# Kernel tuning notes

Hardware: AMD Instinct MI355X
Metric: run time of the kernel (lower is better)

Reference implementation:

```python
import jax, jax.numpy as jnp
import numpy as np

N, D, H, C, ED, E = 50000, 128, 8, 16, 16, 800000  # nodes, model dim, heads, head dim, edge dim, edges

def _layer_norm(x, g, b, eps=1e-5):
    mu = x.mean(-1, keepdims=True)
    var = ((x - mu) ** 2).mean(-1, keepdims=True)
    return (x - mu) * jax.lax.rsqrt(var + eps) * g + b

def setup_inputs() -> dict:
    key = jax.random.key(0)
    ks = jax.random.split(key, 24)
    s = 0.05
    inp = {
        'x': jax.random.normal(ks[0], (N, D), jnp.float32),
        'edge_index': jax.random.randint(ks[1], (2, E), 0, N, jnp.int32),
        'edge_attr': jax.random.normal(ks[2], (E, ED), jnp.float32),
        # TransformerConv params (Linear convention: y = x @ W + b)
        'wq': s * jax.random.normal(ks[3], (D, H * C)), 'bq': s * jax.random.normal(ks[4], (H * C,)),
        'wk': s * jax.random.normal(ks[5], (D, H * C)), 'bk': s * jax.random.normal(ks[6], (H * C,)),
        'wv': s * jax.random.normal(ks[7], (D, H * C)), 'bv': s * jax.random.normal(ks[8], (H * C,)),
        'we': s * jax.random.normal(ks[9], (ED, H * C)),            # lin_edge, bias=False
        'wskip': s * jax.random.normal(ks[10], (D, H * C)), 'bskip': s * jax.random.normal(ks[11], (H * C,)),
        'wbeta': s * jax.random.normal(ks[12], (3 * H * C, 1)),     # lin_beta, bias=False
        # norms
        'ln1_g': 1.0 + s * jax.random.normal(ks[13], (D,)), 'ln1_b': s * jax.random.normal(ks[14], (D,)),
        'ln2_g': 1.0 + s * jax.random.normal(ks[15], (D,)), 'ln2_b': s * jax.random.normal(ks[16], (D,)),
        # FFN
        'w1': s * jax.random.normal(ks[17], (D, 2 * D)), 'b1': s * jax.random.normal(ks[18], (2 * D,)),
        'w2': s * jax.random.normal(ks[19], (2 * D, D)), 'b2': s * jax.random.normal(ks[20], (D,)),
    }
    return inp

def reference(x, edge_index, edge_attr, wq, bq, wk, bk, wv, bv, we, wskip, bskip, wbeta,
              ln1_g, ln1_b, ln2_g, ln2_b, w1, b1, w2, b2):
    src, dst = edge_index[0], edge_index[1]  # message flows src (j) -> dst (i)
    # --- pre-norm + TransformerConv (beta=True, concat=True, eval-mode dropout=identity) ---
    xn = _layer_norm(x, ln1_g, ln1_b)
    q = (xn @ wq + bq).reshape(N, H, C)
    k = (xn @ wk + bk).reshape(N, H, C)
    v = (xn @ wv + bv).reshape(N, H, C)
    e = (edge_attr @ we).reshape(E, H, C)
    kj = k[src] + e                                     # [E,H,C]
    alpha = (q[dst] * kj).sum(-1) / jnp.sqrt(jnp.float32(C))  # [E,H]
    # segment softmax over incoming edges per destination node
    m = jax.ops.segment_max(alpha, dst, num_segments=N)        # [N,H]
    ea = jnp.exp(alpha - m[dst])
    denom = jax.ops.segment_sum(ea, dst, num_segments=N)
    alpha = ea / (denom[dst] + 1e-16)
    msg = (v[src] + e) * alpha[..., None]               # [E,H,C]
    out = jax.ops.segment_sum(msg, dst, num_segments=N).reshape(N, H * C)
    # beta-gated skip
    x_r = xn @ wskip + bskip
    beta = jax.nn.sigmoid(jnp.concatenate([out, x_r, out - x_r], axis=-1) @ wbeta)  # [N,1]
    out = beta * x_r + (1.0 - beta) * out
    x = x + out
    # --- pre-norm FFN ---
    h = _layer_norm(x, ln2_g, ln2_b)
    h = jax.nn.gelu(h @ w1 + b1, approximate=False) @ w2 + b2
    return x + h
```

## Files before the change

kernel.cpp:

```cpp
#include <hip/hip_runtime.h>
#include <math.h>

#define N_NODES 50000
#define D_MODEL 128
#define N_HEADS 8
#define HEAD_C 16
#define E_DIM 16
#define N_EDGES 800000

typedef __attribute__((ext_vector_type(8))) short bf16x8;
typedef __attribute__((ext_vector_type(4))) float f32x4;

__device__ inline ushort f2bf(float f) {
    unsigned u = __float_as_uint(f);
    unsigned r = (u + 0x7fffu + ((u >> 16) & 1u)) >> 16;
    return (ushort)r;
}
__device__ inline float bf2f(ushort h) { return __uint_as_float(((unsigned)h) << 16); }
__device__ inline uint pack2(float a, float b) {
    return (uint)f2bf(a) | ((uint)f2bf(b) << 16);
}

__global__ void prep_weights(const float* __restrict__ wq, const float* __restrict__ wk,
                             const float* __restrict__ wv, const float* __restrict__ wsk,
                             const float* __restrict__ bq, const float* __restrict__ bk,
                             const float* __restrict__ bv, const float* __restrict__ bsk,
                             const float* __restrict__ w1, const float* __restrict__ w2,
                             ushort* __restrict__ wqkvsT, float* __restrict__ bqkvs,
                             ushort* __restrict__ w1T, ushort* __restrict__ w2T)
{
    int idx = blockIdx.x * 256 + threadIdx.x;
    {
        int m = idx >> 7, kk = idx & 127;
        int b = m >> 7, ch = m & 127;
        const float* src = (b == 0) ? wq : (b == 1) ? wk : (b == 2) ? wv : wsk;
        wqkvsT[idx] = f2bf(src[kk * 128 + ch]);
    }
    if (idx < 256 * 128) {
        int m = idx >> 7, k = idx & 127;
        w1T[idx] = f2bf(w1[k * 256 + m]);
    }
    if (idx < 128 * 256) {
        int m = idx >> 8, k = idx & 255;
        w2T[idx] = f2bf(w2[k * 128 + m]);
    }
    if (idx < 512) {
        int b = idx >> 7, ch = idx & 127;
        const float* bb = (b == 0) ? bq : (b == 1) ? bk : (b == 2) ? bv : bsk;
        bqkvs[idx] = bb[ch];
    }
}

__global__ void ln_kernel(const float* __restrict__ in, const float* __restrict__ g,
                          const float* __restrict__ b, ushort* __restrict__ out, int n)
{
    int node = blockIdx.x * 4 + (threadIdx.x >> 6);
    int lane = threadIdx.x & 63;
    if (node >= n) return;
    size_t base = (size_t)node * D_MODEL;
    float v0 = in[base + lane];
    float v1 = in[base + lane + 64];
    float s  = v0 + v1;
    float ss = v0 * v0 + v1 * v1;
    #pragma unroll
    for (int off = 32; off > 0; off >>= 1) {
        s  += __shfl_xor(s,  off, 64);
        ss += __shfl_xor(ss, off, 64);
    }
    float mu  = s * (1.0f / 128.0f);
    float var = ss * (1.0f / 128.0f) - mu * mu;
    float rs  = rsqrtf(var + 1e-5f);
    out[base + lane]      = f2bf((v0 - mu) * rs * g[lane]      + b[lane]);
    out[base + lane + 64] = f2bf((v1 - mu) * rs * g[lane + 64] + b[lane + 64]);
}

__global__ __launch_bounds__(256) void mfma_gemm(
    const ushort* __restrict__ A, const ushort* __restrict__ WT,
    const float* __restrict__ bias, const float* __restrict__ addsrc,
    void* __restrict__ Y, int nrows, int K, int M, int act, int outf32)
{
    __shared__ __align__(16) ushort Al[128 * 128];
    __shared__ __align__(16) ushort Wl[64 * 128];
    int tid = threadIdx.x;
    int wv = tid >> 6, lane = tid & 63;
    int row0 = blockIdx.x * 128;
    int col0 = blockIdx.y * 64;

    f32x4 acc[2][4];
    #pragma unroll
    for (int i = 0; i < 2; ++i)
        #pragma unroll
        for (int j = 0; j < 4; ++j) acc[i][j] = (f32x4){0.f, 0.f, 0.f, 0.f};

    for (int kc = 0; kc < K; kc += 128) {
        __syncthreads();
        #pragma unroll
        for (int i = 0; i < 8; ++i) {
            int c = tid + i * 256;
            int r = c >> 4, c16 = c & 15;
            int gr = row0 + r;
            ulonglong2 val = {0ull, 0ull};
            if (gr < nrows) val = *(const ulonglong2*)(A + (size_t)gr * K + kc + c16 * 8);
            int byte = r * 256 + ((c16 * 16) ^ ((r & 7) << 4));
            *(ulonglong2*)((char*)Al + byte) = val;
        }
        #pragma unroll
        for (int i = 0; i < 4; ++i) {
            int c = tid + i * 256;
            int r = c >> 4, c16 = c & 15;
            ulonglong2 val = *(const ulonglong2*)(WT + (size_t)(col0 + r) * K + kc + c16 * 8);
            int byte = r * 256 + ((c16 * 16) ^ ((r & 7) << 4));
            *(ulonglong2*)((char*)Wl + byte) = val;
        }
        __syncthreads();
        #pragma unroll
        for (int ks = 0; ks < 4; ++ks) {
            bf16x8 af[2], bfr[4];
            #pragma unroll
            for (int rt = 0; rt < 2; ++rt) {
                int r = wv * 32 + rt * 16 + (lane & 15);
                int byte = r * 256 + ((ks * 64 + (lane >> 4) * 16) ^ ((r & 7) << 4));
                af[rt] = *(const bf16x8*)((const char*)Al + byte);
            }
            #pragma unroll
            for (int ct = 0; ct < 4; ++ct) {
                int r = ct * 16 + (lane & 15);
                int byte = r * 256 + ((ks * 64 + (lane >> 4) * 16) ^ ((r & 7) << 4));
                bfr[ct] = *(const bf16x8*)((const char*)Wl + byte);
            }
            #pragma unroll
            for (int rt = 0; rt < 2; ++rt)
                #pragma unroll
                for (int ct = 0; ct < 4; ++ct)
                    acc[rt][ct] = __builtin_amdgcn_mfma_f32_16x16x32_bf16(
                        af[rt], bfr[ct], acc[rt][ct], 0, 0, 0);
        }
    }
    #pragma unroll
    for (int rt = 0; rt < 2; ++rt) {
        #pragma unroll
        for (int ct = 0; ct < 4; ++ct) {
            int gcol = col0 + ct * 16 + (lane & 15);
            float bv = bias[gcol];
            #pragma unroll
            for (int r = 0; r < 4; ++r) {
                int grow = row0 + wv * 32 + rt * 16 + (lane >> 4) * 4 + r;
                if (grow >= nrows) continue;
                float val = acc[rt][ct][r] + bv;
                if (act == 1)
                    val = 0.5f * val * (1.0f + erff(val * 0.70710678118654752f));
                size_t idx = (size_t)grow * M + gcol;
                if (outf32) {
                    float* Yf = (float*)Y;
                    if (addsrc) val += addsrc[idx];
                    Yf[idx] = val;
                } else {
                    ((ushort*)Y)[idx] = f2bf(val);
                }
            }
        }
    }
}

__global__ void hist_kernel(const int* __restrict__ dst, int* __restrict__ deg)
{
    int e = blockIdx.x * 256 + threadIdx.x;
    if (e < N_EDGES) atomicAdd(&deg[dst[e]], 1);
}

__global__ void scan1_kernel(const int* __restrict__ deg, int* __restrict__ off,
                             int* __restrict__ bsum)
{
    __shared__ int sm[256];
    int i = blockIdx.x * 256 + threadIdx.x;
    int v = (i < N_NODES) ? deg[i] : 0;
    sm[threadIdx.x] = v;
    __syncthreads();
    #pragma unroll
    for (int d = 1; d < 256; d <<= 1) {
        int t = (threadIdx.x >= d) ? sm[threadIdx.x - d] : 0;
        __syncthreads();
        sm[threadIdx.x] += t;
        __syncthreads();
    }
    if (i < N_NODES) off[i] = sm[threadIdx.x] - v;
    if (threadIdx.x == 255) bsum[blockIdx.x] = sm[255];
}

__global__ void scan2_kernel(int* __restrict__ bsum, int nb)
{
    __shared__ int sm[256];
    int v = (threadIdx.x < nb) ? bsum[threadIdx.x] : 0;
    sm[threadIdx.x] = v;
    __syncthreads();
    #pragma unroll
    for (int d = 1; d < 256; d <<= 1) {
        int t = (threadIdx.x >= d) ? sm[threadIdx.x - d] : 0;
        __syncthreads();
        sm[threadIdx.x] += t;
        __syncthreads();
    }
    if (threadIdx.x < nb) bsum[threadIdx.x] = sm[threadIdx.x] - v;
}

__global__ void scan3_kernel(int* __restrict__ off, const int* __restrict__ bsum,
                             int* __restrict__ cursor)
{
    int i = blockIdx.x * 256 + threadIdx.x;
    if (i < N_NODES) {
        int o = off[i] + bsum[blockIdx.x];
        off[i] = o;
        cursor[i] = o;
    }
}

__global__ void scatter_kernel(const int* __restrict__ dst, const int* __restrict__ src,
                               const float* __restrict__ eattr, int* __restrict__ cursor,
                               int* __restrict__ src_s, ushort* __restrict__ eattr_s)
{
    int e = blockIdx.x * 256 + threadIdx.x;
    if (e < N_EDGES) {
        int p = atomicAdd(&cursor[dst[e]], 1);
        src_s[p] = src[e];
        const float4* s4 = (const float4*)(eattr + (size_t)e * E_DIM);
        float4 f0 = s4[0], f1 = s4[1], f2 = s4[2], f3 = s4[3];
        uint4 u0, u1;
        u0.x = pack2(f0.x, f0.y); u0.y = pack2(f0.z, f0.w);
        u0.z = pack2(f1.x, f1.y); u0.w = pack2(f1.z, f1.w);
        u1.x = pack2(f2.x, f2.y); u1.y = pack2(f2.z, f2.w);
        u1.z = pack2(f3.x, f3.y); u1.w = pack2(f3.z, f3.w);
        uint4* d4 = (uint4*)(eattr_s + (size_t)p * E_DIM);
        d4[0] = u0; d4[1] = u1;
    }
}

#define ATTN_STEP(P, S, A0, A1, E0, E1) do {                                         \
    int sv_ = src_s[P];                                                              \
    uint eap_ = *(const uint*)(eattr_s + (size_t)(P) * E_DIM + j2);                  \
    float ea0_ = bf2f((ushort)eap_), ea1_ = bf2f((ushort)(eap_ >> 16));              \
    size_t sb_ = (size_t)sv_ * 512;                                                  \
    uint kp_ = *(const uint*)(qkvs + sb_ + 128 + 2 * lane);                          \
    uint vp_ = *(const uint*)(qkvs + sb_ + 256 + 2 * lane);                          \
    float p_ = q0 * bf2f((ushort)kp_) + q1 * bf2f((ushort)(kp_ >> 16))               \
             + ea0_ * qp0 + ea1_ * qp1;                                              \
    p_ += __shfl_xor(p_, 1, 64);                                                     \
    p_ += __shfl_xor(p_, 2, 64);                                                     \
    p_ += __shfl_xor(p_, 4, 64);                                                     \
    float w_ = __expf(fminf(p_ * 0.25f, 60.f));                                      \
    S  += w_;                                                                        \
    A0 += w_ * bf2f((ushort)vp_);                                                    \
    A1 += w_ * bf2f((ushort)(vp_ >> 16));                                            \
    E0 += w_ * ea0_;                                                                 \
    E1 += w_ * ea1_;                                                                 \
} while (0)

__global__ void node_attn(const ushort* __restrict__ qkvs, const float* __restrict__ x,
                          const float* __restrict__ we, const float* __restrict__ wbeta,
                          const int* __restrict__ off, const int* __restrict__ deg,
                          const int* __restrict__ src_s, const ushort* __restrict__ eattr_s,
                          float* __restrict__ xnew)
{
    __shared__ float wl[E_DIM * 128];
    __shared__ float weT[128 * 17];
    __shared__ float sc4[4][128];
    for (int t = threadIdx.x; t < E_DIM * 32; t += 256)
        *(float4*)&wl[t * 4] = *(const float4*)&we[t * 4];
    for (int t = threadIdx.x; t < E_DIM * 128; t += 256) {
        int j = t >> 7, ch = t & 127;
        weT[ch * 17 + j] = we[t];
    }
    __syncthreads();

    int nl   = threadIdx.x >> 6;
    int node = blockIdx.x * 4 + nl;
    int lane = threadIdx.x & 63;
    if (node >= N_NODES) return;

    int j2 = (lane & 7) * 2;
    int hb = (lane >> 3) * 16;

    size_t nb = (size_t)node * 512;
    uint qp = *(const uint*)(qkvs + nb + 2 * lane);
    float q0 = bf2f((ushort)qp), q1 = bf2f((ushort)(qp >> 16));

    sc4[nl][2 * lane]     = q0;
    sc4[nl][2 * lane + 1] = q1;
    float qp0 = 0.f, qp1 = 0.f;
    #pragma unroll
    for (int c = 0; c < 16; ++c) {
        float qc = sc4[nl][hb + c];
        qp0 += qc * weT[(hb + c) * 17 + j2];
        qp1 += qc * weT[(hb + c) * 17 + j2 + 1];
    }

    float SA = 0.f, A0a = 0.f, A1a = 0.f, E0a = 0.f, E1a = 0.f;
    float SB = 0.f, A0b = 0.f, A1b = 0.f, E0b = 0.f, E1b = 0.f;

    int o = off[node], dg = deg[node];
    int i = 0;
    for (; i + 2 <= dg; i += 2) {
        ATTN_STEP(o + i,     SA, A0a, A1a, E0a, E1a);
        ATTN_STEP(o + i + 1, SB, A0b, A1b, E0b, E1b);
    }
    if (i < dg)
        ATTN_STEP(o + i, SA, A0a, A1a, E0a, E1a);

    float S  = SA + SB;
    float A0 = A0a + A0b, A1 = A1a + A1b;
    float E0 = E0a + E0b, E1 = E1a + E1b;

    sc4[nl][2 * lane]     = E0;
    sc4[nl][2 * lane + 1] = E1;
    float ep0 = 0.f, ep1 = 0.f;
    #pragma unroll
    for (int j = 0; j < 16; ++j) {
        float es = sc4[nl][hb + j];
        ep0 += es * wl[j * 128 + 2 * lane];
        ep1 += es * wl[j * 128 + 2 * lane + 1];
    }

    float rinv = 1.f / (S + 1e-16f);
    float o0 = (A0 + ep0) * rinv;
    float o1 = (A1 + ep1) * rinv;

    uint xrp = *(const uint*)(qkvs + nb + 384 + 2 * lane);
    float xr0 = bf2f((ushort)xrp), xr1 = bf2f((ushort)(xrp >> 16));
    float2 wb0 = *(const float2*)&wbeta[2 * lane];
    float2 wb1 = *(const float2*)&wbeta[128 + 2 * lane];
    float2 wb2 = *(const float2*)&wbeta[256 + 2 * lane];
    float dot = o0 * wb0.x + o1 * wb0.y + xr0 * wb1.x + xr1 * wb1.y
              + (o0 - xr0) * wb2.x + (o1 - xr1) * wb2.y;
    #pragma unroll
    for (int w = 32; w > 0; w >>= 1) dot += __shfl_xor(dot, w, 64);
    float beta = 1.f / (1.f + __expf(-dot));

    size_t xb = (size_t)node * D_MODEL + 2 * lane;
    float2 xv = *(const float2*)&x[xb];
    float2 outv;
    outv.x = xv.x + beta * xr0 + (1.f - beta) * o0;
    outv.y = xv.y + beta * xr1 + (1.f - beta) * o1;
    *(float2*)&xnew[xb] = outv;
}

extern "C" void kernel_launch(void* const* d_in, const int* in_sizes, int n_in,
                              void* d_out, int out_size, void* d_ws, size_t ws_size,
                              hipStream_t stream)
{
    const float* x     = (const float*)d_in[0];
    const int*   eidx  = (const int*)  d_in[1];
    const float* eattr = (const float*)d_in[2];
    const float* wq  = (const float*)d_in[3];  const float* bq  = (const float*)d_in[4];
    const float* wk  = (const float*)d_in[5];  const float* bk  = (const float*)d_in[6];
    const float* wv  = (const float*)d_in[7];  const float* bv  = (const float*)d_in[8];
    const float* we  = (const float*)d_in[9];
    const float* wsk = (const float*)d_in[10]; const float* bsk = (const float*)d_in[11];
    const float* wbeta = (const float*)d_in[12];
    const float* ln1g = (const float*)d_in[13]; const float* ln1b = (const float*)d_in[14];
    const float* ln2g = (const float*)d_in[15]; const float* ln2b = (const float*)d_in[16];
    const float* w1 = (const float*)d_in[17]; const float* b1 = (const float*)d_in[18];
    const float* w2 = (const float*)d_in[19]; const float* b2 = (const float*)d_in[20];
    const int* srcp = eidx;
    const int* dstp = eidx + N_EDGES;
    float* out = (float*)d_out;

    char* w = (char*)d_ws;
    size_t o = 0;
    ushort* qkvs_b  = (ushort*)(w + o);
    ushort* hidden_b = qkvs_b;
    o += (size_t)N_NODES * 512 * 2;
    float* xnew = (float*)(w + o);  o += (size_t)N_NODES * 128 * 4;
    ushort* eattr_s = (ushort*)(w + o); o += (size_t)N_EDGES * E_DIM * 2;
    int* src_s = (int*)(w + o);     o += (size_t)N_EDGES * 4;
    ushort* xn_b = (ushort*)(w + o);
    ushort* h2_b = xn_b;
    o += (size_t)N_NODES * 128 * 2;
    ushort* wqkvsT = (ushort*)(w + o); o += 512 * 128 * 2;
    ushort* w1T    = (ushort*)(w + o); o += 256 * 128 * 2;
    ushort* w2T    = (ushort*)(w + o); o += 128 * 256 * 2;
    float*  bqkvs  = (float*)(w + o);  o += 4096;
    int* deg    = (int*)(w + o); o += 200704;
    int* offb   = (int*)(w + o); o += 200704;
    int* cursor = (int*)(w + o); o += 200704;
    int* bsum   = (int*)(w + o); o += 4096;

    dim3 blk(256);
    dim3 lngrid((N_NODES + 3) / 4);
    const int NB = (N_NODES + 255) / 256;
    const int EB = (N_EDGES + 255) / 256;
    const int GB = (N_NODES + 127) / 128;

    prep_weights<<<dim3(256), blk, 0, stream>>>(wq, wk, wv, wsk, bq, bk, bv, bsk,
                                                w1, w2, wqkvsT, bqkvs, w1T, w2T);
    ln_kernel<<<lngrid, blk, 0, stream>>>(x, ln1g, ln1b, xn_b, N_NODES);
    mfma_gemm<<<dim3(GB, 8), blk, 0, stream>>>(xn_b, wqkvsT, bqkvs, nullptr,
                                               qkvs_b, N_NODES, 128, 512, 0, 0);
    hipMemsetAsync(deg, 0, (size_t)N_NODES * 4, stream);
    hist_kernel<<<dim3(EB), blk, 0, stream>>>(dstp, deg);
    scan1_kernel<<<dim3(NB), blk, 0, stream>>>(deg, offb, bsum);
    scan2_kernel<<<dim3(1), blk, 0, stream>>>(bsum, NB);
    scan3_kernel<<<dim3(NB), blk, 0, stream>>>(offb, bsum, cursor);
    scatter_kernel<<<dim3(EB), blk, 0, stream>>>(dstp, srcp, eattr, cursor, src_s, eattr_s);
    node_attn<<<lngrid, blk, 0, stream>>>(qkvs_b, x, we, wbeta, offb, deg,
                                          src_s, eattr_s, xnew);
    ln_kernel<<<lngrid, blk, 0, stream>>>(xnew, ln2g, ln2b, h2_b, N_NODES);
    mfma_gemm<<<dim3(GB, 4), blk, 0, stream>>>(h2_b, w1T, b1, nullptr,
                                               hidden_b, N_NODES, 128, 256, 1, 0);
    mfma_gemm<<<dim3(GB, 2), blk, 0, stream>>>(hidden_b, w2T, b2, xnew,
                                               out, N_NODES, 256, 128, 0, 1);
}
```

Measured before the change: 331.3 us.

## Widen GEMM column tile, scatter packed edge ids, prefetch edges in attention loop

The GEMM tile grows from 128x64 to 128x128 columns, so A tiles are loaded fewer times. This costs more LDS and accumulator registers, which may reduce occupancy. The scatter kernel no longer converts and permutes edge attributes to bf16; it writes packed (src, edge id) pairs, and node_attn gathers fp32 edge_attr directly by original edge id. The attention loop swaps the two-accumulator unroll for a one-ahead software prefetch of K/V/edge data, trading scatter write traffic for random fp32 gathers in the attention kernel.

```diff
diff --git a/kernel.cpp b/kernel.cpp
--- a/kernel.cpp
+++ b/kernel.cpp
@@ -17,9 +17,6 @@
     return (ushort)r;
 }
 __device__ inline float bf2f(ushort h) { return __uint_as_float(((unsigned)h) << 16); }
-__device__ inline uint pack2(float a, float b) {
-    return (uint)f2bf(a) | ((uint)f2bf(b) << 16);
-}
 
 __global__ void prep_weights(const float* __restrict__ wq, const float* __restrict__ wk,
                              const float* __restrict__ wv, const float* __restrict__ wsk,
@@ -80,17 +77,17 @@
     void* __restrict__ Y, int nrows, int K, int M, int act, int outf32)
 {
     __shared__ __align__(16) ushort Al[128 * 128];
-    __shared__ __align__(16) ushort Wl[64 * 128];
+    __shared__ __align__(16) ushort Wl[128 * 128];
     int tid = threadIdx.x;
     int wv = tid >> 6, lane = tid & 63;
     int row0 = blockIdx.x * 128;
-    int col0 = blockIdx.y * 64;
-
-    f32x4 acc[2][4];
+    int col0 = blockIdx.y * 128;
+
+    f32x4 acc[2][8];
     #pragma unroll
     for (int i = 0; i < 2; ++i)
         #pragma unroll
-        for (int j = 0; j < 4; ++j) acc[i][j] = (f32x4){0.f, 0.f, 0.f, 0.f};
+        for (int j = 0; j < 8; ++j) acc[i][j] = (f32x4){0.f, 0.f, 0.f, 0.f};
 
     for (int kc = 0; kc < K; kc += 128) {
         __syncthreads();
@@ -105,7 +102,7 @@
             *(ulonglong2*)((char*)Al + byte) = val;
         }
         #pragma unroll
-        for (int i = 0; i < 4; ++i) {
+        for (int i = 0; i < 8; ++i) {
             int c = tid + i * 256;
             int r = c >> 4, c16 = c & 15;
             ulonglong2 val = *(const ulonglong2*)(WT + (size_t)(col0 + r) * K + kc + c16 * 8);
@@ -115,7 +112,7 @@
         __syncthreads();
         #pragma unroll
         for (int ks = 0; ks < 4; ++ks) {
-            bf16x8 af[2], bfr[4];
+            bf16x8 af[2], bfr[8];
             #pragma unroll
             for (int rt = 0; rt < 2; ++rt) {
                 int r = wv * 32 + rt * 16 + (lane & 15);
@@ -123,7 +120,7 @@
                 af[rt] = *(const bf16x8*)((const char*)Al + byte);
             }
             #pragma unroll
-            for (int ct = 0; ct < 4; ++ct) {
+            for (int ct = 0; ct < 8; ++ct) {
                 int r = ct * 16 + (lane & 15);
                 int byte = r * 256 + ((ks * 64 + (lane >> 4) * 16) ^ ((r & 7) << 4));
                 bfr[ct] = *(const bf16x8*)((const char*)Wl + byte);
@@ -131,7 +128,7 @@
             #pragma unroll
             for (int rt = 0; rt < 2; ++rt)
                 #pragma unroll
-                for (int ct = 0; ct < 4; ++ct)
+                for (int ct = 0; ct < 8; ++ct)
                     acc[rt][ct] = __builtin_amdgcn_mfma_f32_16x16x32_bf16(
                         af[rt], bfr[ct], acc[rt][ct], 0, 0, 0);
         }
@@ -139,7 +136,7 @@
     #pragma unroll
     for (int rt = 0; rt < 2; ++rt) {
         #pragma unroll
-        for (int ct = 0; ct < 4; ++ct) {
+        for (int ct = 0; ct < 8; ++ct) {
             int gcol = col0 + ct * 16 + (lane & 15);
             float bv = bias[gcol];
             #pragma unroll
@@ -215,50 +212,34 @@
 }
 
 __global__ void scatter_kernel(const int* __restrict__ dst, const int* __restrict__ src,
-                               const float* __restrict__ eattr, int* __restrict__ cursor,
-                               int* __restrict__ src_s, ushort* __restrict__ eattr_s)
+                               int* __restrict__ cursor, uint2* __restrict__ pk)
 {
     int e = blockIdx.x * 256 + threadIdx.x;
     if (e < N_EDGES) {
         int p = atomicAdd(&cursor[dst[e]], 1);
-        src_s[p] = src[e];
-        const float4* s4 = (const float4*)(eattr + (size_t)e * E_DIM);
-        float4 f0 = s4[0], f1 = s4[1], f2 = s4[2], f3 = s4[3];
-        uint4 u0, u1;
-        u0.x = pack2(f0.x, f0.y); u0.y = pack2(f0.z, f0.w);
-        u0.z = pack2(f1.x, f1.y); u0.w = pack2(f1.z, f1.w);
-        u1.x = pack2(f2.x, f2.y); u1.y = pack2(f2.z, f2.w);
-        u1.z = pack2(f3.x, f3.y); u1.w = pack2(f3.z, f3.w);
-        uint4* d4 = (uint4*)(eattr_s + (size_t)p * E_DIM);
-        d4[0] = u0; d4[1] = u1;
-    }
-}
-
-#define ATTN_STEP(P, S, A0, A1, E0, E1) do {                                         \
-    int sv_ = src_s[P];                                                              \
-    uint eap_ = *(const uint*)(eattr_s + (size_t)(P) * E_DIM + j2);                  \
-    float ea0_ = bf2f((ushort)eap_), ea1_ = bf2f((ushort)(eap_ >> 16));              \
-    size_t sb_ = (size_t)sv_ * 512;                                                  \
-    uint kp_ = *(const uint*)(qkvs + sb_ + 128 + 2 * lane);                          \
-    uint vp_ = *(const uint*)(qkvs + sb_ + 256 + 2 * lane);                          \
-    float p_ = q0 * bf2f((ushort)kp_) + q1 * bf2f((ushort)(kp_ >> 16))               \
-             + ea0_ * qp0 + ea1_ * qp1;                                              \
+        pk[p] = make_uint2((uint)src[e], (uint)e);
+    }
+}
+
+#define ATTN_COMPUTE(KP, VP, EA) do {                                                \
+    float p_ = q0 * bf2f((ushort)(KP)) + q1 * bf2f((ushort)((KP) >> 16))             \
+             + (EA).x * qp0 + (EA).y * qp1;                                          \
     p_ += __shfl_xor(p_, 1, 64);                                                     \
     p_ += __shfl_xor(p_, 2, 64);                                                     \
     p_ += __shfl_xor(p_, 4, 64);                                                     \
     float w_ = __expf(fminf(p_ * 0.25f, 60.f));                                      \
     S  += w_;                                                                        \
-    A0 += w_ * bf2f((ushort)vp_);                                                    \
-    A1 += w_ * bf2f((ushort)(vp_ >> 16));                                            \
-    E0 += w_ * ea0_;                                                                 \
-    E1 += w_ * ea1_;                                                                 \
+    A0 += w_ * bf2f((ushort)(VP));                                                   \
+    A1 += w_ * bf2f((ushort)((VP) >> 16));                                           \
+    E0 += w_ * (EA).x;                                                               \
+    E1 += w_ * (EA).y;                                                               \
 } while (0)
 
 __global__ void node_attn(const ushort* __restrict__ qkvs, const float* __restrict__ x,
-                          const float* __restrict__ we, const float* __restrict__ wbeta,
+                          const float* __restrict__ eattr, const float* __restrict__ we,
+                          const float* __restrict__ wbeta,
                           const int* __restrict__ off, const int* __restrict__ deg,
-                          const int* __restrict__ src_s, const ushort* __restrict__ eattr_s,
-                          float* __restrict__ xnew)
+                          const uint2* __restrict__ pk, float* __restrict__ xnew)
 {
     __shared__ float wl[E_DIM * 128];
     __shared__ float weT[128 * 17];
@@ -293,21 +274,24 @@
         qp1 += qc * weT[(hb + c) * 17 + j2 + 1];
     }
 
-    float SA = 0.f, A0a = 0.f, A1a = 0.f, E0a = 0.f, E1a = 0.f;
-    float SB = 0.f, A0b = 0.f, A1b = 0.f, E0b = 0.f, E1b = 0.f;
-
+    float S = 0.f, A0 = 0.f, A1 = 0.f, E0 = 0.f, E1 = 0.f;
     int o = off[node], dg = deg[node];
-    int i = 0;
-    for (; i + 2 <= dg; i += 2) {
-        ATTN_STEP(o + i,     SA, A0a, A1a, E0a, E1a);
-        ATTN_STEP(o + i + 1, SB, A0b, A1b, E0b, E1b);
-    }
-    if (i < dg)
-        ATTN_STEP(o + i, SA, A0a, A1a, E0a, E1a);
-
-    float S  = SA + SB;
-    float A0 = A0a + A0b, A1 = A1a + A1b;
-    float E0 = E0a + E0b, E1 = E1a + E1b;
+
+    if (dg > 0) {
+        uint2 se0 = pk[o];
+        uint kp0 = *(const uint*)(qkvs + (size_t)se0.x * 512 + 128 + 2 * lane);
+        uint vp0 = *(const uint*)(qkvs + (size_t)se0.x * 512 + 256 + 2 * lane);
+        float2 ea0 = *(const float2*)(eattr + (size_t)se0.y * E_DIM + j2);
+        for (int i = 1; i < dg; ++i) {
+            uint2 se1 = pk[o + i];
+            uint kp1 = *(const uint*)(qkvs + (size_t)se1.x * 512 + 128 + 2 * lane);
+            uint vp1 = *(const uint*)(qkvs + (size_t)se1.x * 512 + 256 + 2 * lane);
+            float2 ea1 = *(const float2*)(eattr + (size_t)se1.y * E_DIM + j2);
+            ATTN_COMPUTE(kp0, vp0, ea0);
+            kp0 = kp1; vp0 = vp1; ea0 = ea1;
+        }
+        ATTN_COMPUTE(kp0, vp0, ea0);
+    }
 
     sc4[nl][2 * lane]     = E0;
     sc4[nl][2 * lane + 1] = E1;
@@ -369,8 +353,7 @@
     ushort* hidden_b = qkvs_b;
     o += (size_t)N_NODES * 512 * 2;
     float* xnew = (float*)(w + o);  o += (size_t)N_NODES * 128 * 4;
-    ushort* eattr_s = (ushort*)(w + o); o += (size_t)N_EDGES * E_DIM * 2;
-    int* src_s = (int*)(w + o);     o += (size_t)N_EDGES * 4;
+    uint2* pk = (uint2*)(w + o);    o += (size_t)N_EDGES * 8;
     ushort* xn_b = (ushort*)(w + o);
     ushort* h2_b = xn_b;
     o += (size_t)N_NODES * 128 * 2;
@@ -392,19 +375,19 @@
     prep_weights<<<dim3(256), blk, 0, stream>>>(wq, wk, wv, wsk, bq, bk, bv, bsk,
                                                 w1, w2, wqkvsT, bqkvs, w1T, w2T);
     ln_kernel<<<lngrid, blk, 0, stream>>>(x, ln1g, ln1b, xn_b, N_NODES);
-    mfma_gemm<<<dim3(GB, 8), blk, 0, stream>>>(xn_b, wqkvsT, bqkvs, nullptr,
+    mfma_gemm<<<dim3(GB, 4), blk, 0, stream>>>(xn_b, wqkvsT, bqkvs, nullptr,
                                                qkvs_b, N_NODES, 128, 512, 0, 0);
     hipMemsetAsync(deg, 0, (size_t)N_NODES * 4, stream);
     hist_kernel<<<dim3(EB), blk, 0, stream>>>(dstp, deg);
     scan1_kernel<<<dim3(NB), blk, 0, stream>>>(deg, offb, bsum);
     scan2_kernel<<<dim3(1), blk, 0, stream>>>(bsum, NB);
     scan3_kernel<<<dim3(NB), blk, 0, stream>>>(offb, bsum, cursor);
-    scatter_kernel<<<dim3(EB), blk, 0, stream>>>(dstp, srcp, eattr, cursor, src_s, eattr_s);
-    node_attn<<<lngrid, blk, 0, stream>>>(qkvs_b, x, we, wbeta, offb, deg,
-                                          src_s, eattr_s, xnew);
+    scatter_kernel<<<dim3(EB), blk, 0, stream>>>(dstp, srcp, cursor, pk);
+    node_attn<<<lngrid, blk, 0, stream>>>(qkvs_b, x, eattr, we, wbeta, offb, deg,
+                                          pk, xnew);
     ln_kernel<<<lngrid, blk, 0, stream>>>(xnew, ln2g, ln2b, h2_b, N_NODES);
-    mfma_gemm<<<dim3(GB, 4), blk, 0, stream>>>(h2_b, w1T, b1, nullptr,
+    mfma_gemm<<<dim3(GB, 2), blk, 0, stream>>>(h2_b, w1T, b1, nullptr,
                                                hidden_b, N_NODES, 128, 256, 1, 0);
-    mfma_gemm<<<dim3(GB, 2), blk, 0, stream>>>(hidden_b, w2T, b2, xnew,
+    mfma_gemm<<<dim3(GB, 1), blk, 0, stream>>>(hidden_b, w2T, b2, xnew,
                                                out, N_NODES, 256, 128, 0, 1);
 }
```

Result: slower. 409.6 us (+23.6%).
